# Performance work log

Measured on AMD Instinct MI355X. Metric: run time of the kernel, lower is better.

Reference implementation:

```python
import jax, jax.numpy as jnp
import numpy as np

DEPTH = 5

def _path_table(depth):
    # For each leaf, ancestor internal-node index and right/left direction at each of `depth` steps.
    n_internal = 2 ** depth - 1
    n_leaves = 2 ** depth
    anc = np.zeros((n_leaves, depth), dtype=np.int32)
    is_right = np.zeros((n_leaves, depth), dtype=bool)
    for leaf in range(n_leaves):
        node = leaf + n_internal
        for d in range(depth):
            parent = (node - 1) // 2
            anc[leaf, d] = parent
            is_right[leaf, d] = (node % 2 == 0)
            node = parent
    return anc, is_right


def setup_inputs() -> dict:
    key = jax.random.key(0)
    k1, k2, k3 = jax.random.split(key, 3)
    B, F, T = 131072, 128, 20
    n_internal = 2 ** DEPTH - 1
    n_leaves = 2 ** DEPTH
    x = jax.random.normal(k1, (B, F), dtype=jnp.float32)
    split_weights = jax.random.normal(k2, (T, n_internal, F), dtype=jnp.float32) * 0.1
    split_bias = jnp.zeros((T, n_internal), dtype=jnp.float32)
    leaf_logits = jax.random.normal(k3, (T, n_leaves, 2), dtype=jnp.float32) * 0.1
    tree_weights = jnp.ones((T,), dtype=jnp.float32) / T
    # feature masks: fraction 0.7 of features active per tree
    rng = np.random.default_rng(0)
    n_feat_per_tree = max(1, int(F * 0.7))
    masks = np.zeros((T, F), dtype=np.float32)
    for t in range(T):
        idx = rng.permutation(F)[:n_feat_per_tree]
        masks[t, idx] = 1.0
    feature_masks = jnp.asarray(masks)
    return {"x": x, "split_weights": split_weights, "split_bias": split_bias,
            "leaf_logits": leaf_logits, "tree_weights": tree_weights,
            "feature_masks": feature_masks}


def reference(x, split_weights, split_bias, leaf_logits, tree_weights, feature_masks):
    T, N, F = split_weights.shape
    anc, is_right = _path_table(DEPTH)  # static numpy tables [L, DEPTH]
    # Fuse feature masking into the split weights (avoids materializing [T,B,F]).
    Wm = split_weights * feature_masks[:, None, :]           # [T,N,F]
    logits = jnp.einsum('bf,tnf->tbn', x, Wm) + split_bias[:, None, :]
    sp = jax.nn.sigmoid(logits)                              # [T,B,N], temperature = 1.0
    L = N + 1
    leaf_probs = jnp.ones(sp.shape[:2] + (L,), dtype=sp.dtype)  # [T,B,L]
    for d in range(DEPTH):  # small static loop over tree depth
        g = sp[:, :, anc[:, d]]                              # [T,B,L]
        leaf_probs = leaf_probs * jnp.where(is_right[None, None, :, d], g, 1.0 - g)
    leaf_class_probs = jax.nn.softmax(leaf_logits, axis=-1)  # [T,L,2]
    tree_out = jnp.einsum('tbl,tlc->tbc', leaf_probs, leaf_class_probs)
    w = jax.nn.softmax(tree_weights)                         # [T]
    return jnp.einsum('t,tbc->bc', w, tree_out)
```

## Files before the change

kernel.cpp:

```cpp
#include <hip/hip_runtime.h>

typedef __attribute__((ext_vector_type(8))) short bf16x8;
typedef __attribute__((ext_vector_type(4))) float floatx4;

#define T_TREES 20
#define N_NODES 32
#define F_DIM 128
#define M_TILE 128
#define S_SP 36

#define NLOG2E 1.4426950408889634f

__device__ __forceinline__ short f2bf(float f) {
    unsigned u = __float_as_uint(f);
    u += 0x7fffu + ((u >> 16) & 1u);
    return (short)(u >> 16);
}
__device__ __forceinline__ float bf2f(short h) {
    return __uint_as_float(((unsigned)(unsigned short)h) << 16);
}

__device__ __forceinline__ float sig_from_scaled(float u) {
    return __builtin_amdgcn_rcpf(1.f + __builtin_amdgcn_exp2f(u));
}

__global__ void nrf_prep(const float* __restrict__ sw, const float* __restrict__ sb,
                         const float* __restrict__ ll, const float* __restrict__ tw,
                         const float* __restrict__ fm,
                         short* __restrict__ w_all, float* __restrict__ bias_p,
                         float* __restrict__ lv0) {
    int t = blockIdx.x, slice = blockIdx.y, tid = threadIdx.x;

    const float* fmt = fm + t * F_DIM;
    const float* swt = sw + t * 31 * F_DIM;
    int idx = slice * 512 + tid;
    #pragma unroll
    for (int r = 0; r < 2; ++r, idx += 256) {
        int n = idx >> 7, f = idx & 127;
        short wb = (n < 31 && fmt[f] != 0.f) ? f2bf(swt[n * F_DIM + f]) : (short)0;
        w_all[t * (N_NODES * F_DIM) + idx] = wb;
    }

    if (slice == 0) {
        __shared__ float tws[T_TREES];
        if (tid < T_TREES) tws[tid] = tw[tid];
        __syncthreads();
        if (tid < N_NODES) {
            float m = -1e30f;
            for (int i = 0; i < T_TREES; ++i) m = fmaxf(m, bf2f(f2bf(tws[i])));
            float s = 0.f;
            for (int i = 0; i < T_TREES; ++i) s += __expf(bf2f(f2bf(tws[i])) - m);
            float wt = __expf(bf2f(f2bf(tws[t])) - m) / s;

            float bv = (tid < 31) ? bf2f(f2bf(sb[t * 31 + tid])) : 0.f;
            bias_p[t * N_NODES + tid] = bv * (-NLOG2E);
            float a  = bf2f(f2bf(ll[(t * 32 + tid) * 2 + 0]));
            float bb = bf2f(f2bf(ll[(t * 32 + tid) * 2 + 1]));
            float mx = fmaxf(a, bb);
            float e0 = __expf(a - mx), e1 = __expf(bb - mx);
            lv0[t * N_NODES + tid] = wt * e0 / (e0 + e1);
        }
    }
}

__global__ __launch_bounds__(256, 4) void nrf_main(const float* __restrict__ x,
        const short* __restrict__ w_all, const float* __restrict__ bias_p,
        const float* __restrict__ lv0, float* __restrict__ out) {
    __shared__ short bstage[2][N_NODES * F_DIM];
    __shared__ float sp_all[4][N_NODES * S_SP];
    __shared__ float lv_s[T_TREES * N_NODES];
    __shared__ float bias_s[T_TREES * N_NODES];

    int tid = threadIdx.x;
    int wave = tid >> 6, lane = tid & 63;
    int q = lane >> 4, c16 = lane & 15;

    for (int i = tid; i < T_TREES * N_NODES; i += 256) { lv_s[i] = lv0[i]; bias_s[i] = bias_p[i]; }

    float* spb = sp_all[wave];
    int rowBase = blockIdx.x * M_TILE + wave * 32;

    bf16x8 afrag[2][4];
    #pragma unroll
    for (int mi = 0; mi < 2; ++mi) {
        const float* xr = x + (size_t)(rowBase + mi * 16 + c16) * F_DIM;
        #pragma unroll
        for (int ks = 0; ks < 4; ++ks) {
            const float4* p = (const float4*)(xr + ks * 32 + q * 8);
            float4 f0 = p[0], f1 = p[1];
            bf16x8 v;
            v[0]=f2bf(f0.x); v[1]=f2bf(f0.y); v[2]=f2bf(f0.z); v[3]=f2bf(f0.w);
            v[4]=f2bf(f1.x); v[5]=f2bf(f1.y); v[6]=f2bf(f1.z); v[7]=f2bf(f1.w);
            afrag[mi][ks] = v;
        }
    }

    const unsigned soff0 = (unsigned)(tid * 32) ^ ((unsigned)((tid >> 3) & 7) << 4);
    const bf16x8* wsrc = (const bf16x8*)w_all + tid * 2;

    {
        bf16x8 s0 = wsrc[0], s1 = wsrc[1];
        *(bf16x8*)((char*)bstage[0] + soff0) = s0;
        *(bf16x8*)((char*)bstage[0] + (soff0 ^ 16u)) = s1;
    }

    int s = lane & 15, h = lane >> 4;
    int s_node = 3 + h;
    float acc0 = 0.f, acc1 = 0.f;
    __syncthreads();

    #pragma unroll
    for (int t = 0; t < T_TREES; ++t) {
        const int cur = t & 1, nxt = cur ^ 1;
        bf16x8 pf0, pf1;
        if (t + 1 < T_TREES) {
            const bf16x8* src = (const bf16x8*)(w_all + (t + 1) * (N_NODES * F_DIM)) + tid * 2;
            pf0 = src[0]; pf1 = src[1];
        }

        bf16x8 bfrag[2][4];
        const char* bb = (const char*)bstage[cur];
        #pragma unroll
        for (int ni = 0; ni < 2; ++ni) {
            unsigned row = (unsigned)(ni * 16 + c16);
            unsigned swz = (row & 7u) << 4;
            #pragma unroll
            for (int ks = 0; ks < 4; ++ks) {
                unsigned lin = row * 256u + (unsigned)(ks * 64 + q * 16);
                bfrag[ni][ks] = *(const bf16x8*)(bb + (lin ^ swz));
            }
        }

        floatx4 acc[2][2];
        #pragma unroll
        for (int mi = 0; mi < 2; ++mi)
            #pragma unroll
            for (int ni = 0; ni < 2; ++ni)
                acc[mi][ni] = (floatx4){0.f,0.f,0.f,0.f};
        #pragma unroll
        for (int ks = 0; ks < 4; ++ks)
            #pragma unroll
            for (int mi = 0; mi < 2; ++mi)
                #pragma unroll
                for (int ni = 0; ni < 2; ++ni)
                    acc[mi][ni] = __builtin_amdgcn_mfma_f32_16x16x32_bf16(
                        afrag[mi][ks], bfrag[ni][ks], acc[mi][ni], 0, 0, 0);

        #pragma unroll
        for (int ni = 0; ni < 2; ++ni) {
            int col = ni * 16 + c16;
            float bv = bias_s[t * N_NODES + col];
            #pragma unroll
            for (int mi = 0; mi < 2; ++mi) {
                float4 v;
                v.x = sig_from_scaled(fmaf(acc[mi][ni][0], -NLOG2E, bv));
                v.y = sig_from_scaled(fmaf(acc[mi][ni][1], -NLOG2E, bv));
                v.z = sig_from_scaled(fmaf(acc[mi][ni][2], -NLOG2E, bv));
                v.w = sig_from_scaled(fmaf(acc[mi][ni][3], -NLOG2E, bv));
                *(float4*)&spb[col * S_SP + mi * 16 + q * 4] = v;
            }
        }
        float g0a = spb[s],                          g0b = spb[s + 16];
        int n1 = 1 + (h >> 1);
        float g1a = spb[n1 * S_SP + s],              g1b = spb[n1 * S_SP + s + 16];
        float g2a = spb[s_node * S_SP + s],          g2b = spb[s_node * S_SP + s + 16];
        int n3a = 2 * s_node + 1, n3b = 2 * s_node + 2;
        float g3aa = spb[n3a * S_SP + s],            g3ab = spb[n3a * S_SP + s + 16];
        float g3ba = spb[n3b * S_SP + s],            g3bb = spb[n3b * S_SP + s + 16];
        int n4 = 4 * s_node + 3;
        float g4aa = spb[n4 * S_SP + s],             g4ab = spb[n4 * S_SP + s + 16];
        float g4ba = spb[(n4+1) * S_SP + s],         g4bb = spb[(n4+1) * S_SP + s + 16];
        float g4ca = spb[(n4+2) * S_SP + s],         g4cb = spb[(n4+2) * S_SP + s + 16];
        float g4da = spb[(n4+3) * S_SP + s],         g4db = spb[(n4+3) * S_SP + s + 16];

        const float* lvt = &lv_s[t * N_NODES + h * 8];

        {
            float f0 = (h & 2) ? g0a : 1.f - g0a;
            float f1 = (h & 1) ? g1a : 1.f - g1a;
            float pre = f0 * f1;
            float p1 = pre * g2a, p0 = pre - p1;
            float q1 = p0 * g3aa, q0 = p0 - q1;
            float q3 = p1 * g3ba, q2 = p1 - q3;
            float r1 = q0 * g4aa, r0 = q0 - r1;
            float r3 = q1 * g4ba, r2 = q1 - r3;
            float r5 = q2 * g4ca, r4 = q2 - r5;
            float r7 = q3 * g4da, r6 = q3 - r7;
            acc0 += r0*lvt[0] + r1*lvt[1] + r2*lvt[2] + r3*lvt[3]
                  + r4*lvt[4] + r5*lvt[5] + r6*lvt[6] + r7*lvt[7];
        }
        {
            float f0 = (h & 2) ? g0b : 1.f - g0b;
            float f1 = (h & 1) ? g1b : 1.f - g1b;
            float pre = f0 * f1;
            float p1 = pre * g2b, p0 = pre - p1;
            float q1 = p0 * g3ab, q0 = p0 - q1;
            float q3 = p1 * g3bb, q2 = p1 - q3;
            float r1 = q0 * g4ab, r0 = q0 - r1;
            float r3 = q1 * g4bb, r2 = q1 - r3;
            float r5 = q2 * g4cb, r4 = q2 - r5;
            float r7 = q3 * g4db, r6 = q3 - r7;
            acc1 += r0*lvt[0] + r1*lvt[1] + r2*lvt[2] + r3*lvt[3]
                  + r4*lvt[4] + r5*lvt[5] + r6*lvt[6] + r7*lvt[7];
        }

        if (t + 1 < T_TREES) {
            *(bf16x8*)((char*)bstage[nxt] + soff0) = pf0;
            *(bf16x8*)((char*)bstage[nxt] + (soff0 ^ 16u)) = pf1;
        }
        __syncthreads();
    }

    acc0 += __shfl_xor(acc0, 16, 64);
    acc0 += __shfl_xor(acc0, 32, 64);
    acc1 += __shfl_xor(acc1, 16, 64);
    acc1 += __shfl_xor(acc1, 32, 64);
    if (h == 0) {
        float2 o0; o0.x = acc0; o0.y = 1.f - acc0;
        *(float2*)(out + (size_t)(rowBase + s) * 2) = o0;
        float2 o1; o1.x = acc1; o1.y = 1.f - acc1;
        *(float2*)(out + (size_t)(rowBase + 16 + s) * 2) = o1;
    }
}

extern "C" void kernel_launch(void* const* d_in, const int* in_sizes, int n_in,
                              void* d_out, int out_size, void* d_ws, size_t ws_size,
                              hipStream_t stream) {
    const float* x  = (const float*)d_in[0];
    const float* sw = (const float*)d_in[1];
    const float* sb = (const float*)d_in[2];
    const float* ll = (const float*)d_in[3];
    const float* tw = (const float*)d_in[4];
    const float* fm = (const float*)d_in[5];
    float* out = (float*)d_out;

    short* w_all  = (short*)d_ws;
    float* bias_p = (float*)((char*)d_ws + 163840);
    float* lv0    = (float*)((char*)d_ws + 166400);

    dim3 pgrid(T_TREES, 8);
    nrf_prep<<<pgrid, 256, 0, stream>>>(sw, sb, ll, tw, fm, w_all, bias_p, lv0);

    int B = in_sizes[0] / F_DIM;
    nrf_main<<<B / M_TILE, 256, 0, stream>>>(x, w_all, bias_p, lv0, out);
}
```

Baseline: 140.3 us.

## Split work across 8 waves of 16 rows each instead of 4 waves of 32

Doubles the block to 512 threads so each wave handles one 16-row MFMA tile instead of two. This halves per-thread registers and fragments and lets each thread load one 16-byte weight chunk per tree instead of two. The sigmoid scratch layout is re-padded for the narrower tile. The intent is more waves in flight to hide global-load and LDS latency, at the cost of more waves per block sharing each weight-staging barrier and less reuse of B fragments read from LDS per wave.

```diff
diff --git a/kernel.cpp b/kernel.cpp
--- a/kernel.cpp
+++ b/kernel.cpp
@@ -7,7 +7,8 @@
 #define N_NODES 32
 #define F_DIM 128
 #define M_TILE 128
-#define S_SP 36
+#define THREADS 512
+#define S_SP2 17
 
 #define NLOG2E 1.4426950408889634f
 
@@ -63,11 +64,11 @@
     }
 }
 
-__global__ __launch_bounds__(256, 4) void nrf_main(const float* __restrict__ x,
+__global__ __launch_bounds__(THREADS, 8) void nrf_main(const float* __restrict__ x,
         const short* __restrict__ w_all, const float* __restrict__ bias_p,
         const float* __restrict__ lv0, float* __restrict__ out) {
     __shared__ short bstage[2][N_NODES * F_DIM];
-    __shared__ float sp_all[4][N_NODES * S_SP];
+    __shared__ float sp_all[8][N_NODES * S_SP2];
     __shared__ float lv_s[T_TREES * N_NODES];
     __shared__ float bias_s[T_TREES * N_NODES];
 
@@ -75,15 +76,14 @@
     int wave = tid >> 6, lane = tid & 63;
     int q = lane >> 4, c16 = lane & 15;
 
-    for (int i = tid; i < T_TREES * N_NODES; i += 256) { lv_s[i] = lv0[i]; bias_s[i] = bias_p[i]; }
+    for (int i = tid; i < T_TREES * N_NODES; i += THREADS) { lv_s[i] = lv0[i]; bias_s[i] = bias_p[i]; }
 
     float* spb = sp_all[wave];
-    int rowBase = blockIdx.x * M_TILE + wave * 32;
-
-    bf16x8 afrag[2][4];
-    #pragma unroll
-    for (int mi = 0; mi < 2; ++mi) {
-        const float* xr = x + (size_t)(rowBase + mi * 16 + c16) * F_DIM;
+    int rowBase = blockIdx.x * M_TILE + wave * 16;
+
+    bf16x8 afrag[4];
+    {
+        const float* xr = x + (size_t)(rowBase + c16) * F_DIM;
         #pragma unroll
         for (int ks = 0; ks < 4; ++ks) {
             const float4* p = (const float4*)(xr + ks * 32 + q * 8);
@@ -91,32 +91,28 @@
             bf16x8 v;
             v[0]=f2bf(f0.x); v[1]=f2bf(f0.y); v[2]=f2bf(f0.z); v[3]=f2bf(f0.w);
             v[4]=f2bf(f1.x); v[5]=f2bf(f1.y); v[6]=f2bf(f1.z); v[7]=f2bf(f1.w);
-            afrag[mi][ks] = v;
-        }
-    }
-
-    const unsigned soff0 = (unsigned)(tid * 32) ^ ((unsigned)((tid >> 3) & 7) << 4);
-    const bf16x8* wsrc = (const bf16x8*)w_all + tid * 2;
+            afrag[ks] = v;
+        }
+    }
+
+    const unsigned soff = (unsigned)(tid * 16) ^ ((unsigned)((tid >> 4) & 7u) << 4);
 
     {
-        bf16x8 s0 = wsrc[0], s1 = wsrc[1];
-        *(bf16x8*)((char*)bstage[0] + soff0) = s0;
-        *(bf16x8*)((char*)bstage[0] + (soff0 ^ 16u)) = s1;
+        bf16x8 s0 = ((const bf16x8*)w_all)[tid];
+        *(bf16x8*)((char*)bstage[0] + soff) = s0;
     }
 
     int s = lane & 15, h = lane >> 4;
     int s_node = 3 + h;
-    float acc0 = 0.f, acc1 = 0.f;
+    float acc0 = 0.f;
     __syncthreads();
 
     #pragma unroll
     for (int t = 0; t < T_TREES; ++t) {
         const int cur = t & 1, nxt = cur ^ 1;
-        bf16x8 pf0, pf1;
-        if (t + 1 < T_TREES) {
-            const bf16x8* src = (const bf16x8*)(w_all + (t + 1) * (N_NODES * F_DIM)) + tid * 2;
-            pf0 = src[0]; pf1 = src[1];
-        }
+        bf16x8 pf;
+        if (t + 1 < T_TREES)
+            pf = ((const bf16x8*)(w_all + (t + 1) * (N_NODES * F_DIM)))[tid];
 
         bf16x8 bfrag[2][4];
         const char* bb = (const char*)bstage[cur];
@@ -131,95 +127,61 @@
             }
         }
 
-        floatx4 acc[2][2];
-        #pragma unroll
-        for (int mi = 0; mi < 2; ++mi)
+        floatx4 acc[2];
+        acc[0] = (floatx4){0.f,0.f,0.f,0.f};
+        acc[1] = (floatx4){0.f,0.f,0.f,0.f};
+        #pragma unroll
+        for (int ks = 0; ks < 4; ++ks)
             #pragma unroll
             for (int ni = 0; ni < 2; ++ni)
-                acc[mi][ni] = (floatx4){0.f,0.f,0.f,0.f};
-        #pragma unroll
-        for (int ks = 0; ks < 4; ++ks)
-            #pragma unroll
-            for (int mi = 0; mi < 2; ++mi)
-                #pragma unroll
-                for (int ni = 0; ni < 2; ++ni)
-                    acc[mi][ni] = __builtin_amdgcn_mfma_f32_16x16x32_bf16(
-                        afrag[mi][ks], bfrag[ni][ks], acc[mi][ni], 0, 0, 0);
+                acc[ni] = __builtin_amdgcn_mfma_f32_16x16x32_bf16(
+                    afrag[ks], bfrag[ni][ks], acc[ni], 0, 0, 0);
 
         #pragma unroll
         for (int ni = 0; ni < 2; ++ni) {
             int col = ni * 16 + c16;
             float bv = bias_s[t * N_NODES + col];
             #pragma unroll
-            for (int mi = 0; mi < 2; ++mi) {
-                float4 v;
-                v.x = sig_from_scaled(fmaf(acc[mi][ni][0], -NLOG2E, bv));
-                v.y = sig_from_scaled(fmaf(acc[mi][ni][1], -NLOG2E, bv));
-                v.z = sig_from_scaled(fmaf(acc[mi][ni][2], -NLOG2E, bv));
-                v.w = sig_from_scaled(fmaf(acc[mi][ni][3], -NLOG2E, bv));
-                *(float4*)&spb[col * S_SP + mi * 16 + q * 4] = v;
-            }
-        }
-        float g0a = spb[s],                          g0b = spb[s + 16];
+            for (int j = 0; j < 4; ++j)
+                spb[col * S_SP2 + q * 4 + j] =
+                    sig_from_scaled(fmaf(acc[ni][j], -NLOG2E, bv));
+        }
+        float g0 = spb[s];
         int n1 = 1 + (h >> 1);
-        float g1a = spb[n1 * S_SP + s],              g1b = spb[n1 * S_SP + s + 16];
-        float g2a = spb[s_node * S_SP + s],          g2b = spb[s_node * S_SP + s + 16];
+        float g1 = spb[n1 * S_SP2 + s];
+        float g2 = spb[s_node * S_SP2 + s];
         int n3a = 2 * s_node + 1, n3b = 2 * s_node + 2;
-        float g3aa = spb[n3a * S_SP + s],            g3ab = spb[n3a * S_SP + s + 16];
-        float g3ba = spb[n3b * S_SP + s],            g3bb = spb[n3b * S_SP + s + 16];
+        float g3a = spb[n3a * S_SP2 + s], g3b = spb[n3b * S_SP2 + s];
         int n4 = 4 * s_node + 3;
-        float g4aa = spb[n4 * S_SP + s],             g4ab = spb[n4 * S_SP + s + 16];
-        float g4ba = spb[(n4+1) * S_SP + s],         g4bb = spb[(n4+1) * S_SP + s + 16];
-        float g4ca = spb[(n4+2) * S_SP + s],         g4cb = spb[(n4+2) * S_SP + s + 16];
-        float g4da = spb[(n4+3) * S_SP + s],         g4db = spb[(n4+3) * S_SP + s + 16];
+        float g4a = spb[n4 * S_SP2 + s],       g4b = spb[(n4+1) * S_SP2 + s];
+        float g4c = spb[(n4+2) * S_SP2 + s],   g4d = spb[(n4+3) * S_SP2 + s];
 
         const float* lvt = &lv_s[t * N_NODES + h * 8];
-
         {
-            float f0 = (h & 2) ? g0a : 1.f - g0a;
-            float f1 = (h & 1) ? g1a : 1.f - g1a;
+            float f0 = (h & 2) ? g0 : 1.f - g0;
+            float f1 = (h & 1) ? g1 : 1.f - g1;
             float pre = f0 * f1;
-            float p1 = pre * g2a, p0 = pre - p1;
-            float q1 = p0 * g3aa, q0 = p0 - q1;
-            float q3 = p1 * g3ba, q2 = p1 - q3;
-            float r1 = q0 * g4aa, r0 = q0 - r1;
-            float r3 = q1 * g4ba, r2 = q1 - r3;
-            float r5 = q2 * g4ca, r4 = q2 - r5;
-            float r7 = q3 * g4da, r6 = q3 - r7;
+            float p1 = pre * g2, p0 = pre - p1;
+            float q1 = p0 * g3a, q0 = p0 - q1;
+            float q3 = p1 * g3b, q2 = p1 - q3;
+            float r1 = q0 * g4a, r0 = q0 - r1;
+            float r3 = q1 * g4b, r2 = q1 - r3;
+            float r5 = q2 * g4c, r4 = q2 - r5;
+            float r7 = q3 * g4d, r6 = q3 - r7;
             acc0 += r0*lvt[0] + r1*lvt[1] + r2*lvt[2] + r3*lvt[3]
                   + r4*lvt[4] + r5*lvt[5] + r6*lvt[6] + r7*lvt[7];
         }
-        {
-            float f0 = (h & 2) ? g0b : 1.f - g0b;
-            float f1 = (h & 1) ? g1b : 1.f - g1b;
-            float pre = f0 * f1;
-            float p1 = pre * g2b, p0 = pre - p1;
-            float q1 = p0 * g3ab, q0 = p0 - q1;
-            float q3 = p1 * g3bb, q2 = p1 - q3;
-            float r1 = q0 * g4ab, r0 = q0 - r1;
-            float r3 = q1 * g4bb, r2 = q1 - r3;
-            float r5 = q2 * g4cb, r4 = q2 - r5;
-            float r7 = q3 * g4db, r6 = q3 - r7;
-            acc1 += r0*lvt[0] + r1*lvt[1] + r2*lvt[2] + r3*lvt[3]
-                  + r4*lvt[4] + r5*lvt[5] + r6*lvt[6] + r7*lvt[7];
-        }
-
-        if (t + 1 < T_TREES) {
-            *(bf16x8*)((char*)bstage[nxt] + soff0) = pf0;
-            *(bf16x8*)((char*)bstage[nxt] + (soff0 ^ 16u)) = pf1;
-        }
+
+        if (t + 1 < T_TREES)
+            *(bf16x8*)((char*)bstage[nxt] + soff) = pf;
         __syncthreads();
     }
 
     acc0 += __shfl_xor(acc0, 16, 64);
     acc0 += __shfl_xor(acc0, 32, 64);
-    acc1 += __shfl_xor(acc1, 16, 64);
-    acc1 += __shfl_xor(acc1, 32, 64);
     if (h == 0) {
-        float2 o0; o0.x = acc0; o0.y = 1.f - acc0;
-        *(float2*)(out + (size_t)(rowBase + s) * 2) = o0;
-        float2 o1; o1.x = acc1; o1.y = 1.f - acc1;
-        *(float2*)(out + (size_t)(rowBase + 16 + s) * 2) = o1;
+        float2 o; o.x = acc0; o.y = 1.f - acc0;
+        *(float2*)(out + (size_t)(rowBase + s) * 2) = o;
     }
 }
 
@@ -242,5 +204,5 @@
     nrf_prep<<<pgrid, 256, 0, stream>>>(sw, sb, ll, tw, fm, w_all, bias_p, lv0);
 
     int B = in_sizes[0] / F_DIM;
-    nrf_main<<<B / M_TILE, 256, 0, stream>>>(x, w_all, bias_p, lv0, out);
-}
+    nrf_main<<<B / M_TILE, THREADS, 0, stream>>>(x, w_all, bias_p, lv0, out);
+}
```

Measured after the change: 256.2 us. 1.83x slower.
